# Optimization experiments

Measured on AMD Instinct MI355X. Metric: run time of the kernel, lower is better.

Reference implementation:

```python
import jax, jax.numpy as jnp
import numpy as np

B, S, D, H, E, K = 4, 2048, 1024, 2048, 8, 2
GH = max(D // 2, 32)  # 512 gating hidden


def setup_inputs() -> dict:
    key = jax.random.key(0)
    ks = jax.random.split(key, 16)
    def xav(k, shape):
        fan_in, fan_out = shape[0], shape[1]
        lim = (6.0 / (fan_in + fan_out)) ** 0.5
        return jax.random.uniform(k, shape, jnp.float32, -lim, lim)
    return {
        'x': jax.random.normal(ks[0], (B, S, D), jnp.float32),
        'feature_types': jax.random.randint(ks[1], (B, S), 0, 3),
        'gw1': xav(ks[2], (D, GH)), 'gb1': jnp.zeros((GH,), jnp.float32),
        'gw2': xav(ks[3], (GH, GH // 2)), 'gb2': jnp.zeros((GH // 2,), jnp.float32),
        'gw3': xav(ks[4], (GH // 2, E)), 'gb3': jnp.zeros((E,), jnp.float32),
        'type_emb': jax.random.normal(ks[5], (3, GH // 4), jnp.float32),
        'tw': xav(ks[6], (GH // 4, E)), 'tb': jnp.zeros((E,), jnp.float32),
        'ew': jax.random.normal(ks[7], (E, D, H), jnp.float32) * (1.0 / D ** 0.5),
        'eb': jnp.zeros((E, H), jnp.float32),
        'ow': xav(ks[8], (H, D)), 'ob': jnp.zeros((D,), jnp.float32),
    }


def reference(x, feature_types, gw1, gb1, gw2, gb2, gw3, gb3, type_emb, tw, tb, ew, eb, ow, ob):
    # Gating network (eval mode: dropout = identity)
    h = jax.nn.relu(x @ gw1 + gb1)
    h = jax.nn.relu(h @ gw2 + gb2)
    gate_logits = h @ gw3 + gb3                      # [B,S,E]
    type_bias = type_emb[feature_types] @ tw + tb    # [B,S,E]
    gate_weights = jax.nn.softmax(gate_logits + type_bias, axis=-1)

    # Top-k routing, renormalize selected weights
    expert_weights, expert_indices = jax.lax.top_k(gate_weights, K)  # [B,S,K]
    expert_weights = expert_weights / expert_weights.sum(-1, keepdims=True)

    # Dense expert compute (faithful to original: every expert on every token)
    expert_outputs = jnp.einsum('bsd,edh->bseh', x, ew) + eb         # [B,S,E,H]

    # Gather selected experts and combine
    sel = jnp.take_along_axis(expert_outputs, expert_indices[..., None], axis=2)  # [B,S,K,H]
    output = jnp.sum(expert_weights[..., None] * sel, axis=2)        # [B,S,H]

    output = jax.nn.relu(output)
    return output @ ow + ob                                          # [B,S,D]
```

## Files before the change

kernel.cpp:

```cpp
#include <hip/hip_runtime.h>

#define T_TOK 8192
#define DDIM 1024
#define GH1 512
#define GH2 256
#define NEXP 8
#define HDIM 2048

typedef __attribute__((ext_vector_type(8))) short short8;
typedef __attribute__((ext_vector_type(4))) float f32x4;

__device__ __forceinline__ unsigned short f2bf(float f) {
    unsigned int u = __float_as_uint(f);
    u += 0x7fffu + ((u >> 16) & 1u);
    return (unsigned short)(u >> 16);
}
__device__ __forceinline__ float bf2f(unsigned short h) {
    return __uint_as_float(((unsigned int)h) << 16);
}

__device__ __forceinline__ void async16(const void* g, void* l) {
#if __has_builtin(__builtin_amdgcn_global_load_lds)
    __builtin_amdgcn_global_load_lds((const __attribute__((address_space(1))) void*)g,
                                     (__attribute__((address_space(3))) void*)l, 16, 0, 0);
#else
    *(uint4*)l = *(const uint4*)g;
#endif
}

__global__ __launch_bounds__(256)
void f2b_kernel(const float* __restrict__ in, unsigned short* __restrict__ out)
{
    size_t i = ((size_t)blockIdx.x * 256 + threadIdx.x) * 8;
    float4 a = *(const float4*)(in + i);
    float4 b = *(const float4*)(in + i + 4);
    uint4 r;
    r.x = (unsigned)f2bf(a.x) | ((unsigned)f2bf(a.y) << 16);
    r.y = (unsigned)f2bf(a.z) | ((unsigned)f2bf(a.w) << 16);
    r.z = (unsigned)f2bf(b.x) | ((unsigned)f2bf(b.y) << 16);
    r.w = (unsigned)f2bf(b.z) | ((unsigned)f2bf(b.w) << 16);
    *(uint4*)(out + i) = r;
}

__global__ __launch_bounds__(256)
void transpose_f2b(const float* __restrict__ in, unsigned short* __restrict__ out,
                   int R, int C, int tilesC, int ntile)
{
    int bid = blockIdx.x;
    int z = bid / ntile;
    int r = bid - z * ntile;
    int tr = r / tilesC, tc = r - tr * tilesC;
    const float* ib = in + (size_t)z * R * C;
    unsigned short* ob = out + (size_t)z * R * C;
    __shared__ float lds[32][33];
    int t = threadIdx.x;
    int i = t >> 3, j4 = (t & 7) << 2;
    float4 v = *(const float4*)(ib + (size_t)(tr * 32 + i) * C + tc * 32 + j4);
    lds[i][j4 + 0] = v.x;
    lds[i][j4 + 1] = v.y;
    lds[i][j4 + 2] = v.z;
    lds[i][j4 + 3] = v.w;
    __syncthreads();
    ushort4 o;
    o.x = f2bf(lds[j4 + 0][i]);
    o.y = f2bf(lds[j4 + 1][i]);
    o.z = f2bf(lds[j4 + 2][i]);
    o.w = f2bf(lds[j4 + 3][i]);
    *(ushort4*)(ob + (size_t)(tc * 32 + i) * R + tr * 32 + j4) = o;
}

__global__ __launch_bounds__(256)
void sgemm_relu_128x64(const float* __restrict__ A, const float* __restrict__ B,
                       const float* __restrict__ bias, float* __restrict__ C,
                       int N, int Kd, int nbn)
{
    int bid = blockIdx.x;
    int bm = bid / nbn, bn = bid - bm * nbn;
    __shared__ float As[16][128];
    __shared__ float Bs[16][64];
    int t = threadIdx.x;
    int tx = t & 15, ty = t >> 4;
    float acc[8][4];
#pragma unroll
    for (int i = 0; i < 8; ++i)
#pragma unroll
        for (int j = 0; j < 4; ++j) acc[i][j] = 0.f;

    int arow = t >> 1, akk = (t & 1) << 3;
    int bkk = t >> 4, bcol = (t & 15) << 2;
    const float* aptr = A + (size_t)(bm * 128 + arow) * Kd + akk;
    const float* bptr = B + (size_t)bkk * N + bn * 64 + bcol;

    for (int k0 = 0; k0 < Kd; k0 += 16) {
        float4 a0 = *(const float4*)(aptr + k0);
        float4 a1 = *(const float4*)(aptr + k0 + 4);
        float4 bv = *(const float4*)(bptr + (size_t)k0 * N);
        __syncthreads();
        As[akk + 0][arow] = a0.x;
        As[akk + 1][arow] = a0.y;
        As[akk + 2][arow] = a0.z;
        As[akk + 3][arow] = a0.w;
        As[akk + 4][arow] = a1.x;
        As[akk + 5][arow] = a1.y;
        As[akk + 6][arow] = a1.z;
        As[akk + 7][arow] = a1.w;
        *(float4*)&Bs[bkk][bcol] = bv;
        __syncthreads();
#pragma unroll
        for (int kk = 0; kk < 16; ++kk) {
            float a[8], b[4];
            *(float4*)&a[0] = *(const float4*)&As[kk][ty * 8];
            *(float4*)&a[4] = *(const float4*)&As[kk][ty * 8 + 4];
            *(float4*)&b[0] = *(const float4*)&Bs[kk][tx * 4];
#pragma unroll
            for (int i = 0; i < 8; ++i)
#pragma unroll
                for (int j = 0; j < 4; ++j)
                    acc[i][j] = fmaf(a[i], b[j], acc[i][j]);
        }
    }
#pragma unroll
    for (int i = 0; i < 8; ++i) {
        int row = bm * 128 + ty * 8 + i;
        float4 o;
        float* op = &o.x;
#pragma unroll
        for (int j = 0; j < 4; ++j) {
            float v = acc[i][j] + bias[bn * 64 + tx * 4 + j];
            op[j] = v > 0.f ? v : 0.f;
        }
        *(float4*)&C[(size_t)row * N + bn * 64 + tx * 4] = o;
    }
}

__global__ __launch_bounds__(256)
void sgemm_relu(const float* __restrict__ A, const float* __restrict__ B,
                const float* __restrict__ bias, float* __restrict__ C,
                int N, int Kd, int nbn)
{
    int bid = blockIdx.x;
    int bm = bid / nbn, bn = bid - bm * nbn;
    __shared__ float As[16][64];
    __shared__ float Bs[16][64];
    int t = threadIdx.x;
    int tx = t & 15, ty = t >> 4;
    float acc[4][4];
#pragma unroll
    for (int i = 0; i < 4; ++i)
#pragma unroll
        for (int j = 0; j < 4; ++j) acc[i][j] = 0.f;

    int arow = t >> 2, akk = (t & 3) << 2;
    int bkk = t >> 4, bcol = (t & 15) << 2;
    const float* aptr = A + (size_t)(bm * 64 + arow) * Kd + akk;
    const float* bptr = B + (size_t)bkk * N + bn * 64 + bcol;

    for (int k0 = 0; k0 < Kd; k0 += 16) {
        float4 av = *(const float4*)(aptr + k0);
        float4 bv = *(const float4*)(bptr + (size_t)k0 * N);
        __syncthreads();
        As[akk + 0][arow] = av.x;
        As[akk + 1][arow] = av.y;
        As[akk + 2][arow] = av.z;
        As[akk + 3][arow] = av.w;
        *(float4*)&Bs[bkk][bcol] = bv;
        __syncthreads();
#pragma unroll
        for (int kk = 0; kk < 16; ++kk) {
            float a[4], b[4];
            *(float4*)&a[0] = *(const float4*)&As[kk][ty * 4];
            *(float4*)&b[0] = *(const float4*)&Bs[kk][tx * 4];
#pragma unroll
            for (int i = 0; i < 4; ++i)
#pragma unroll
                for (int j = 0; j < 4; ++j)
                    acc[i][j] = fmaf(a[i], b[j], acc[i][j]);
        }
    }
#pragma unroll
    for (int i = 0; i < 4; ++i) {
        int row = bm * 64 + ty * 4 + i;
        float4 o;
        float* op = &o.x;
#pragma unroll
        for (int j = 0; j < 4; ++j) {
            float v = acc[i][j] + bias[bn * 64 + tx * 4 + j];
            op[j] = v > 0.f ? v : 0.f;
        }
        *(float4*)&C[(size_t)row * N + bn * 64 + tx * 4] = o;
    }
}

__global__ __launch_bounds__(256)
void gate_tail(const float* __restrict__ h2, const int* __restrict__ ftyp,
               const float* __restrict__ gw3, const float* __restrict__ gb3,
               const float* __restrict__ temb, const float* __restrict__ tw,
               const float* __restrict__ tb,
               int* __restrict__ eidx, float* __restrict__ ewt)
{
    __shared__ float sw3[GH2 * NEXP];
    __shared__ float stw[128 * NEXP];
    __shared__ float ste[3 * 128];
    int t = threadIdx.x;
    for (int i = t; i < GH2 * NEXP; i += 256) sw3[i] = gw3[i];
    for (int i = t; i < 128 * NEXP; i += 256) stw[i] = tw[i];
    for (int i = t; i < 3 * 128; i += 256) ste[i] = temb[i];
    __syncthreads();
    int tok = blockIdx.x * 256 + t;
    float lg[NEXP];
#pragma unroll
    for (int e = 0; e < NEXP; ++e) lg[e] = gb3[e] + tb[e];
    const float* hrow = h2 + (size_t)tok * GH2;
    for (int k = 0; k < GH2; k += 4) {
        float4 hv = *(const float4*)(hrow + k);
        float hvv[4] = {hv.x, hv.y, hv.z, hv.w};
#pragma unroll
        for (int j = 0; j < 4; ++j) {
            float v = hvv[j];
#pragma unroll
            for (int e = 0; e < NEXP; ++e)
                lg[e] = fmaf(v, sw3[(k + j) * NEXP + e], lg[e]);
        }
    }
    int ft = ftyp[tok];
    const float* te = ste + ft * 128;
    for (int k = 0; k < 128; k += 4) {
#pragma unroll
        for (int j = 0; j < 4; ++j) {
            float v = te[k + j];
#pragma unroll
            for (int e = 0; e < NEXP; ++e)
                lg[e] = fmaf(v, stw[(k + j) * NEXP + e], lg[e]);
        }
    }
    int a0 = 0; float b0 = lg[0];
#pragma unroll
    for (int e = 1; e < NEXP; ++e) if (lg[e] > b0) { b0 = lg[e]; a0 = e; }
    int a1 = -1; float b1 = -3.4e38f;
#pragma unroll
    for (int e = 0; e < NEXP; ++e) if (e != a0 && lg[e] > b1) { b1 = lg[e]; a1 = e; }
    float w0 = 1.f / (1.f + expf(b1 - b0));
    eidx[tok * 2 + 0] = a0;
    eidx[tok * 2 + 1] = a1;
    ewt[tok * 2 + 0] = w0;
    ewt[tok * 2 + 1] = 1.f - w0;
}

__global__ __launch_bounds__(256)
void route_kernel(const int* __restrict__ eidx, int* __restrict__ cnt,
                  int* __restrict__ entries)
{
    int tok = blockIdx.x * 256 + threadIdx.x;
#pragma unroll
    for (int k = 0; k < 2; ++k) {
        int e = eidx[tok * 2 + k];
        int p = atomicAdd(&cnt[e], 1);
        entries[e * T_TOK + p] = (tok << 1) | k;
    }
}

template<int GATHER>
__global__ __launch_bounds__(256)
void bgemm(const unsigned short* __restrict__ A, const unsigned short* __restrict__ BT,
           const float* __restrict__ bias, float* __restrict__ Cf,
           unsigned short* __restrict__ Y0, unsigned short* __restrict__ Y1,
           const int* __restrict__ entries, const int* __restrict__ cnt,
           int N, int Kd, int nbm, int nbn)
{
    int bid = blockIdx.x;
    int e = 0, bm, bn, cntE = 0;
    const unsigned short* Bt = BT;
    const float* bs = bias;
    if (GATHER) {
        e = bid & (NEXP - 1);
        int r = bid >> 3;
        bm = r / nbn; bn = r - bm * nbn;
        cntE = cnt[e];
        if (bm * 128 >= cntE) return;
        Bt = BT + (size_t)e * HDIM * DDIM;
        bs = bias + e * HDIM;
    } else {
        bm = bid / nbn; bn = bid - bm * nbn;
    }

    __shared__ __align__(16) unsigned short As[2][128 * 32];
    __shared__ __align__(16) unsigned short Bs[2][128 * 32];
    __shared__ int rowtok[128];

    int t = threadIdx.x;
    if (GATHER) {
        if (t < 128) {
            int idx = bm * 128 + t;
            rowtok[t] = entries[(size_t)e * T_TOK + bm * 128 + ((idx < cntE) ? t : 0)];
        }
        __syncthreads();
    }

    int arow0 = t >> 2;
    int kkA = (t & 3) << 3;
    const unsigned short *asrc0, *asrc1;
    if (GATHER) {
        asrc0 = A + (size_t)(rowtok[arow0] >> 1) * Kd + kkA;
        asrc1 = A + (size_t)(rowtok[arow0 + 64] >> 1) * Kd + kkA;
    } else {
        asrc0 = A + (size_t)(bm * 128 + arow0) * Kd + kkA;
        asrc1 = A + (size_t)(bm * 128 + arow0 + 64) * Kd + kkA;
    }
    const unsigned short* bsrc0 = Bt + (size_t)(bn * 128 + arow0) * Kd + kkA;
    const unsigned short* bsrc1 = Bt + (size_t)(bn * 128 + arow0 + 64) * Kd + kkA;

    int lane = t & 63, wave = t >> 6;
    int wr = (wave >> 1) * 64, wc = (wave & 1) * 64;
    int l15 = lane & 15, lhi = lane >> 4;

    f32x4 zero = {0.f, 0.f, 0.f, 0.f};
    f32x4 acc[4][4];
#pragma unroll
    for (int m = 0; m < 4; ++m)
#pragma unroll
        for (int n = 0; n < 4; ++n) acc[m][n] = zero;

    auto STAGE = [&](int buf, int k0) {
        async16(asrc0 + k0, &As[buf][t * 8]);
        async16(asrc1 + k0, &As[buf][t * 8 + 2048]);
        async16(bsrc0 + k0, &Bs[buf][t * 8]);
        async16(bsrc1 + k0, &Bs[buf][t * 8 + 2048]);
    };

    STAGE(0, 0);
    STAGE(1, 32);
    asm volatile("s_waitcnt vmcnt(4)" ::: "memory");
    __builtin_amdgcn_s_barrier();

    int nt = Kd >> 5;
    int cur = 0;
    for (int kt = 0; kt < nt; ++kt) {
        short8 af[4], bf[4];
#pragma unroll
        for (int m = 0; m < 4; ++m)
            af[m] = *(const short8*)&As[cur][(wr + m * 16 + l15) * 32 + lhi * 8];
#pragma unroll
        for (int n = 0; n < 4; ++n)
            bf[n] = *(const short8*)&Bs[cur][(wc + n * 16 + l15) * 32 + lhi * 8];
#pragma unroll
        for (int m = 0; m < 4; ++m)
#pragma unroll
            for (int n = 0; n < 4; ++n)
                acc[m][n] = __builtin_amdgcn_mfma_f32_16x16x32_bf16(af[m], bf[n], acc[m][n], 0, 0, 0);
        if (kt + 1 < nt) {
            asm volatile("s_waitcnt lgkmcnt(0)" ::: "memory");
            __builtin_amdgcn_s_barrier();
            if (kt + 2 < nt) {
                STAGE(cur, (kt + 2) << 5);
                asm volatile("s_waitcnt vmcnt(4)" ::: "memory");
            } else {
                asm volatile("s_waitcnt vmcnt(0)" ::: "memory");
            }
            __builtin_amdgcn_s_barrier();
            cur ^= 1;
        }
    }

    if (GATHER) {
#pragma unroll
        for (int m = 0; m < 4; ++m) {
            int rl = wr + m * 16 + lhi * 4;
#pragma unroll
            for (int q = 0; q < 4; ++q) {
                int gidx = bm * 128 + rl + q;
                if (gidx < cntE) {
                    int ent = rowtok[rl + q];
                    unsigned short* Y = (ent & 1) ? Y1 : Y0;
                    size_t rowoff = (size_t)(ent >> 1) * HDIM;
#pragma unroll
                    for (int n = 0; n < 4; ++n) {
                        int col = bn * 128 + wc + n * 16 + l15;
                        Y[rowoff + col] = f2bf(acc[m][n][q] + bs[col]);
                    }
                }
            }
        }
    } else {
#pragma unroll
        for (int m = 0; m < 4; ++m) {
            int row = bm * 128 + wr + m * 16 + lhi * 4;
#pragma unroll
            for (int n = 0; n < 4; ++n) {
                int col = bn * 128 + wc + n * 16 + l15;
                float bv = bs[col];
#pragma unroll
                for (int q = 0; q < 4; ++q)
                    Cf[(size_t)(row + q) * N + col] = acc[m][n][q] + bv;
            }
        }
    }
}

__global__ __launch_bounds__(256)
void combine_kernel(const unsigned short* __restrict__ Y0,
                    const unsigned short* __restrict__ Y1,
                    const float* __restrict__ wts,
                    unsigned short* __restrict__ Hc)
{
    size_t i = (size_t)blockIdx.x * 256 + threadIdx.x;
    size_t base = i * 8;
    int tok = (int)(base >> 11);
    float w0 = wts[tok * 2], w1 = wts[tok * 2 + 1];
    uint4 a = *(const uint4*)(Y0 + base);
    uint4 b = *(const uint4*)(Y1 + base);
    unsigned int ain[4] = {a.x, a.y, a.z, a.w};
    unsigned int bin[4] = {b.x, b.y, b.z, b.w};
    unsigned int r[4];
#pragma unroll
    for (int q = 0; q < 4; ++q) {
        float v0 = w0 * bf2f((unsigned short)(ain[q] & 0xffff)) +
                   w1 * bf2f((unsigned short)(bin[q] & 0xffff));
        float v1 = w0 * bf2f((unsigned short)(ain[q] >> 16)) +
                   w1 * bf2f((unsigned short)(bin[q] >> 16));
        v0 = v0 > 0.f ? v0 : 0.f;
        v1 = v1 > 0.f ? v1 : 0.f;
        r[q] = (unsigned int)f2bf(v0) | ((unsigned int)f2bf(v1) << 16);
    }
    uint4 o = {r[0], r[1], r[2], r[3]};
    *(uint4*)(Hc + base) = o;
}

extern "C" void kernel_launch(void* const* d_in, const int* in_sizes, int n_in,
                              void* d_out, int out_size, void* d_ws, size_t ws_size,
                              hipStream_t stream)
{
    const float* x    = (const float*)d_in[0];
    const int*   ftyp = (const int*)d_in[1];
    const float* gw1  = (const float*)d_in[2];
    const float* gb1  = (const float*)d_in[3];
    const float* gw2  = (const float*)d_in[4];
    const float* gb2  = (const float*)d_in[5];
    const float* gw3  = (const float*)d_in[6];
    const float* gb3  = (const float*)d_in[7];
    const float* temb = (const float*)d_in[8];
    const float* tw   = (const float*)d_in[9];
    const float* tb   = (const float*)d_in[10];
    const float* ew   = (const float*)d_in[11];
    const float* eb   = (const float*)d_in[12];
    const float* ow   = (const float*)d_in[13];
    const float* ob   = (const float*)d_in[14];
    float* out = (float*)d_out;

    char* p = (char*)d_ws;
    auto alloc = [&](size_t bytes) {
        char* r = p;
        p += (bytes + 255) & ~(size_t)255;
        return r;
    };
    unsigned short* xb  = (unsigned short*)alloc((size_t)T_TOK * DDIM * 2);
    float* h1           = (float*)alloc((size_t)T_TOK * GH1 * 4);
    float* h2           = (float*)alloc((size_t)T_TOK * GH2 * 4);
    int* eidx           = (int*)alloc((size_t)T_TOK * 2 * 4);
    float* ewt          = (float*)alloc((size_t)T_TOK * 2 * 4);
    int* cnt            = (int*)alloc(256);
    int* entries        = (int*)alloc((size_t)NEXP * T_TOK * 4);
    unsigned short* ewT = (unsigned short*)alloc((size_t)NEXP * HDIM * DDIM * 2);
    unsigned short* owT = (unsigned short*)alloc((size_t)DDIM * HDIM * 2);
    unsigned short* Y0  = (unsigned short*)alloc((size_t)T_TOK * HDIM * 2);
    unsigned short* Y1  = (unsigned short*)alloc((size_t)T_TOK * HDIM * 2);
    unsigned short* Hc  = (unsigned short*)alloc((size_t)T_TOK * HDIM * 2);

    hipMemsetAsync(cnt, 0, 256, stream);
    f2b_kernel<<<(T_TOK * DDIM / 8) / 256, 256, 0, stream>>>(x, xb);
    transpose_f2b<<<NEXP * 32 * 64, 256, 0, stream>>>(ew, ewT, DDIM, HDIM, 64, 32 * 64);
    transpose_f2b<<<64 * 32, 256, 0, stream>>>(ow, owT, HDIM, DDIM, 32, 64 * 32);

    sgemm_relu_128x64<<<64 * 8, 256, 0, stream>>>(x, gw1, gb1, h1, GH1, DDIM, 8);
    sgemm_relu<<<128 * 4, 256, 0, stream>>>(h1, gw2, gb2, h2, GH2, GH1, 4);
    gate_tail<<<T_TOK / 256, 256, 0, stream>>>(h2, ftyp, gw3, gb3, temb, tw, tb, eidx, ewt);
    route_kernel<<<T_TOK / 256, 256, 0, stream>>>(eidx, cnt, entries);

    bgemm<1><<<NEXP * 64 * 16, 256, 0, stream>>>(xb, ewT, eb, nullptr, Y0, Y1,
                                                 entries, cnt, HDIM, DDIM, 64, 16);
    combine_kernel<<<(T_TOK * HDIM / 8) / 256, 256, 0, stream>>>(Y0, Y1, ewt, Hc);
    bgemm<0><<<64 * 8, 256, 0, stream>>>(Hc, owT, ob, out, nullptr, nullptr,
                                         nullptr, nullptr, DDIM, HDIM, 64, 8);
}
```

Before: 677.4 us.

## Use persistent work-stealing grouped GEMM for MoE expert layer

Replaces the grid-per-tile gathered expert GEMM with a persistent kernel of 1024 blocks. Each block grabs chunks from a per-expert atomic counter and computes two adjacent N-tiles per chunk, reusing the gathered row-token list. This is meant to avoid launching many blocks that exit early for empty expert tiles and to cut gather setup per tile. Blocks stay pinned to one expert (blockIdx & 7), so an uneven expert load can leave some blocks idle while others run long. The A tile is also reloaded for the second N-tile.

```diff
diff --git a/kernel.cpp b/kernel.cpp
--- a/kernel.cpp
+++ b/kernel.cpp
@@ -259,6 +259,124 @@
     }
 }
 
+__global__ __launch_bounds__(256)
+void bgemm_moe(const unsigned short* __restrict__ A, const unsigned short* __restrict__ BT,
+               const float* __restrict__ bias,
+               unsigned short* __restrict__ Y0, unsigned short* __restrict__ Y1,
+               const int* __restrict__ entries, const int* __restrict__ cnt,
+               int* __restrict__ wctr)
+{
+    int e = blockIdx.x & (NEXP - 1);
+    const unsigned short* Bt = BT + (size_t)e * HDIM * DDIM;
+    const float* bs = bias + e * HDIM;
+    int cntE = cnt[e];
+    int nchunks = ((cntE + 127) >> 7) << 3;
+
+    __shared__ __align__(16) unsigned short As[2][128 * 32];
+    __shared__ __align__(16) unsigned short Bs[2][128 * 32];
+    __shared__ int rowtok[128];
+    __shared__ int cidx_s;
+
+    int t = threadIdx.x;
+    int lane = t & 63, wave = t >> 6;
+    int wr = (wave >> 1) * 64, wc = (wave & 1) * 64;
+    int l15 = lane & 15, lhi = lane >> 4;
+    int arow0 = t >> 2, kkA = (t & 3) << 3;
+    f32x4 zero = {0.f, 0.f, 0.f, 0.f};
+
+    for (;;) {
+        __syncthreads();
+        if (t == 0) cidx_s = atomicAdd(&wctr[e], 1);
+        __syncthreads();
+        int c = cidx_s;
+        if (c >= nchunks) break;
+        int bm = c >> 3, bn0 = (c & 7) << 1;
+
+        if (t < 128) {
+            int idx = bm * 128 + t;
+            rowtok[t] = entries[(size_t)e * T_TOK + bm * 128 + ((idx < cntE) ? t : 0)];
+        }
+        __syncthreads();
+        const unsigned short* asrc0 = A + (size_t)(rowtok[arow0] >> 1) * DDIM + kkA;
+        const unsigned short* asrc1 = A + (size_t)(rowtok[arow0 + 64] >> 1) * DDIM + kkA;
+
+        for (int bi = 0; bi < 2; ++bi) {
+            if (bi) __syncthreads();
+            int bn = bn0 + bi;
+            const unsigned short* bsrc0 = Bt + (size_t)(bn * 128 + arow0) * DDIM + kkA;
+            const unsigned short* bsrc1 = Bt + (size_t)(bn * 128 + arow0 + 64) * DDIM + kkA;
+
+            f32x4 acc[4][4];
+#pragma unroll
+            for (int m = 0; m < 4; ++m)
+#pragma unroll
+                for (int n = 0; n < 4; ++n) acc[m][n] = zero;
+
+            async16(asrc0, &As[0][t * 8]);
+            async16(asrc1, &As[0][t * 8 + 2048]);
+            async16(bsrc0, &Bs[0][t * 8]);
+            async16(bsrc1, &Bs[0][t * 8 + 2048]);
+            async16(asrc0 + 32, &As[1][t * 8]);
+            async16(asrc1 + 32, &As[1][t * 8 + 2048]);
+            async16(bsrc0 + 32, &Bs[1][t * 8]);
+            async16(bsrc1 + 32, &Bs[1][t * 8 + 2048]);
+            asm volatile("s_waitcnt vmcnt(4)" ::: "memory");
+            __builtin_amdgcn_s_barrier();
+
+            int cur = 0;
+            for (int kt = 0; kt < 32; ++kt) {
+                short8 af[4], bf[4];
+#pragma unroll
+                for (int m = 0; m < 4; ++m)
+                    af[m] = *(const short8*)&As[cur][(wr + m * 16 + l15) * 32 + lhi * 8];
+#pragma unroll
+                for (int n = 0; n < 4; ++n)
+                    bf[n] = *(const short8*)&Bs[cur][(wc + n * 16 + l15) * 32 + lhi * 8];
+#pragma unroll
+                for (int m = 0; m < 4; ++m)
+#pragma unroll
+                    for (int n = 0; n < 4; ++n)
+                        acc[m][n] = __builtin_amdgcn_mfma_f32_16x16x32_bf16(af[m], bf[n], acc[m][n], 0, 0, 0);
+                if (kt + 1 < 32) {
+                    asm volatile("s_waitcnt lgkmcnt(0)" ::: "memory");
+                    __builtin_amdgcn_s_barrier();
+                    if (kt + 2 < 32) {
+                        int k0 = (kt + 2) << 5;
+                        async16(asrc0 + k0, &As[cur][t * 8]);
+                        async16(asrc1 + k0, &As[cur][t * 8 + 2048]);
+                        async16(bsrc0 + k0, &Bs[cur][t * 8]);
+                        async16(bsrc1 + k0, &Bs[cur][t * 8 + 2048]);
+                        asm volatile("s_waitcnt vmcnt(4)" ::: "memory");
+                    } else {
+                        asm volatile("s_waitcnt vmcnt(0)" ::: "memory");
+                    }
+                    __builtin_amdgcn_s_barrier();
+                    cur ^= 1;
+                }
+            }
+
+#pragma unroll
+            for (int m = 0; m < 4; ++m) {
+                int rl = wr + m * 16 + lhi * 4;
+#pragma unroll
+                for (int q = 0; q < 4; ++q) {
+                    int gidx = bm * 128 + rl + q;
+                    if (gidx < cntE) {
+                        int ent = rowtok[rl + q];
+                        unsigned short* Y = (ent & 1) ? Y1 : Y0;
+                        size_t rowoff = (size_t)(ent >> 1) * HDIM;
+#pragma unroll
+                        for (int n = 0; n < 4; ++n) {
+                            int col = bn * 128 + wc + n * 16 + l15;
+                            Y[rowoff + col] = f2bf(acc[m][n][q] + bs[col]);
+                        }
+                    }
+                }
+            }
+        }
+    }
+}
+
 template<int GATHER>
 __global__ __launch_bounds__(256)
 void bgemm(const unsigned short* __restrict__ A, const unsigned short* __restrict__ BT,
@@ -268,44 +386,18 @@
            int N, int Kd, int nbm, int nbn)
 {
     int bid = blockIdx.x;
-    int e = 0, bm, bn, cntE = 0;
+    int bm = bid / nbn, bn = bid - bm * nbn;
     const unsigned short* Bt = BT;
     const float* bs = bias;
-    if (GATHER) {
-        e = bid & (NEXP - 1);
-        int r = bid >> 3;
-        bm = r / nbn; bn = r - bm * nbn;
-        cntE = cnt[e];
-        if (bm * 128 >= cntE) return;
-        Bt = BT + (size_t)e * HDIM * DDIM;
-        bs = bias + e * HDIM;
-    } else {
-        bm = bid / nbn; bn = bid - bm * nbn;
-    }
 
     __shared__ __align__(16) unsigned short As[2][128 * 32];
     __shared__ __align__(16) unsigned short Bs[2][128 * 32];
-    __shared__ int rowtok[128];
 
     int t = threadIdx.x;
-    if (GATHER) {
-        if (t < 128) {
-            int idx = bm * 128 + t;
-            rowtok[t] = entries[(size_t)e * T_TOK + bm * 128 + ((idx < cntE) ? t : 0)];
-        }
-        __syncthreads();
-    }
-
     int arow0 = t >> 2;
     int kkA = (t & 3) << 3;
-    const unsigned short *asrc0, *asrc1;
-    if (GATHER) {
-        asrc0 = A + (size_t)(rowtok[arow0] >> 1) * Kd + kkA;
-        asrc1 = A + (size_t)(rowtok[arow0 + 64] >> 1) * Kd + kkA;
-    } else {
-        asrc0 = A + (size_t)(bm * 128 + arow0) * Kd + kkA;
-        asrc1 = A + (size_t)(bm * 128 + arow0 + 64) * Kd + kkA;
-    }
+    const unsigned short* asrc0 = A + (size_t)(bm * 128 + arow0) * Kd + kkA;
+    const unsigned short* asrc1 = A + (size_t)(bm * 128 + arow0 + 64) * Kd + kkA;
     const unsigned short* bsrc0 = Bt + (size_t)(bn * 128 + arow0) * Kd + kkA;
     const unsigned short* bsrc1 = Bt + (size_t)(bn * 128 + arow0 + 64) * Kd + kkA;
 
@@ -361,37 +453,16 @@
         }
     }
 
-    if (GATHER) {
-#pragma unroll
-        for (int m = 0; m < 4; ++m) {
-            int rl = wr + m * 16 + lhi * 4;
-#pragma unroll
-            for (int q = 0; q < 4; ++q) {
-                int gidx = bm * 128 + rl + q;
-                if (gidx < cntE) {
-                    int ent = rowtok[rl + q];
-                    unsigned short* Y = (ent & 1) ? Y1 : Y0;
-                    size_t rowoff = (size_t)(ent >> 1) * HDIM;
-#pragma unroll
-                    for (int n = 0; n < 4; ++n) {
-                        int col = bn * 128 + wc + n * 16 + l15;
-                        Y[rowoff + col] = f2bf(acc[m][n][q] + bs[col]);
-                    }
-                }
-            }
-        }
-    } else {
-#pragma unroll
-        for (int m = 0; m < 4; ++m) {
-            int row = bm * 128 + wr + m * 16 + lhi * 4;
-#pragma unroll
-            for (int n = 0; n < 4; ++n) {
-                int col = bn * 128 + wc + n * 16 + l15;
-                float bv = bs[col];
-#pragma unroll
-                for (int q = 0; q < 4; ++q)
-                    Cf[(size_t)(row + q) * N + col] = acc[m][n][q] + bv;
-            }
+#pragma unroll
+    for (int m = 0; m < 4; ++m) {
+        int row = bm * 128 + wr + m * 16 + lhi * 4;
+#pragma unroll
+        for (int n = 0; n < 4; ++n) {
+            int col = bn * 128 + wc + n * 16 + l15;
+            float bv = bs[col];
+#pragma unroll
+            for (int q = 0; q < 4; ++q)
+                Cf[(size_t)(row + q) * N + col] = acc[m][n][q] + bv;
         }
     }
 }
@@ -458,6 +529,7 @@
     int* eidx           = (int*)alloc((size_t)T_TOK * 2 * 4);
     float* ewt          = (float*)alloc((size_t)T_TOK * 2 * 4);
     int* cnt            = (int*)alloc(256);
+    int* wctr           = (int*)alloc(256);
     int* entries        = (int*)alloc((size_t)NEXP * T_TOK * 4);
     unsigned short* ewT = (unsigned short*)alloc((size_t)NEXP * HDIM * DDIM * 2);
     unsigned short* owT = (unsigned short*)alloc((size_t)DDIM * HDIM * 2);
@@ -465,7 +537,7 @@
     unsigned short* Y1  = (unsigned short*)alloc((size_t)T_TOK * HDIM * 2);
     unsigned short* Hc  = (unsigned short*)alloc((size_t)T_TOK * HDIM * 2);
 
-    hipMemsetAsync(cnt, 0, 256, stream);
+    hipMemsetAsync(cnt, 0, 512, stream);
     f2b_kernel<<<(T_TOK * DDIM / 8) / 256, 256, 0, stream>>>(x, xb);
     transpose_f2b<<<NEXP * 32 * 64, 256, 0, stream>>>(ew, ewT, DDIM, HDIM, 64, 32 * 64);
     transpose_f2b<<<64 * 32, 256, 0, stream>>>(ow, owT, HDIM, DDIM, 32, 64 * 32);
@@ -475,8 +547,7 @@
     gate_tail<<<T_TOK / 256, 256, 0, stream>>>(h2, ftyp, gw3, gb3, temb, tw, tb, eidx, ewt);
     route_kernel<<<T_TOK / 256, 256, 0, stream>>>(eidx, cnt, entries);
 
-    bgemm<1><<<NEXP * 64 * 16, 256, 0, stream>>>(xb, ewT, eb, nullptr, Y0, Y1,
-                                                 entries, cnt, HDIM, DDIM, 64, 16);
+    bgemm_moe<<<1024, 256, 0, stream>>>(xb, ewT, eb, Y0, Y1, entries, cnt, wctr);
     combine_kernel<<<(T_TOK * HDIM / 8) / 256, 256, 0, stream>>>(Y0, Y1, ewt, Hc);
     bgemm<0><<<64 * 8, 256, 0, stream>>>(Hc, owT, ob, out, nullptr, nullptr,
                                          nullptr, nullptr, DDIM, HDIM, 64, 8);
```

Measured after the change: 693.5 us. 1.02x slower.
